# Performance work log

Hardware: AMD Instinct MI355X
Metric: run time of the kernel (lower is better)

Reference implementation:

```python
import jax, jax.numpy as jnp
import numpy as np

N_NODES = 50000
N_EDGES = 800000
IN_C, HID_C, OUT_C = 128, 128, 1


def setup_inputs() -> dict:
    key = jax.random.key(0)
    ks = jax.random.split(key, 10)
    x = jax.random.normal(ks[0], (N_NODES, IN_C), dtype=jnp.float32)
    x2 = jax.random.normal(ks[1], (1,), dtype=jnp.float32)
    edge_index = jax.random.randint(ks[2], (2, N_EDGES), 0, N_NODES, dtype=jnp.int64)
    # GCNConv params (glorot-ish scale) and final linear
    W1 = jax.random.normal(ks[3], (IN_C, HID_C), dtype=jnp.float32) / np.sqrt(IN_C)
    b1 = jnp.zeros((HID_C,), dtype=jnp.float32)
    W2 = jax.random.normal(ks[4], (HID_C, HID_C), dtype=jnp.float32) / np.sqrt(HID_C)
    b2 = jnp.zeros((HID_C,), dtype=jnp.float32)
    Wlin = jax.random.normal(ks[5], (HID_C, OUT_C), dtype=jnp.float32) / np.sqrt(HID_C)
    blin = jnp.zeros((OUT_C,), dtype=jnp.float32)
    return {"x": x, "x2": x2, "edge_index": edge_index, "num_nodes": N_NODES,
            "W1": W1, "b1": b1, "W2": W2, "b2": b2, "Wlin": Wlin, "blin": blin}


def _gcn_conv(h, W, b, src, dst, norm, num_nodes):
    # linear transform then normalized scatter-add aggregation (PyG GCNConv)
    h = h @ W  # [N, C_out]
    msg = h[src] * norm[:, None]  # gather + scale, [E+N, C_out]
    out = jax.ops.segment_sum(msg, dst, num_segments=num_nodes)
    return out + b


def _gcn_norm(edge_index, num_nodes):
    # add self-loops, compute sym-normalization coefficients D^-1/2 A D^-1/2
    loop = jnp.arange(num_nodes, dtype=edge_index.dtype)
    src = jnp.concatenate([edge_index[0], loop])
    dst = jnp.concatenate([edge_index[1], loop])
    ones = jnp.ones(src.shape[0], dtype=jnp.float32)
    deg = jax.ops.segment_sum(ones, dst, num_segments=num_nodes)
    dinv = jnp.where(deg > 0, jax.lax.rsqrt(deg), 0.0)
    norm = dinv[src] * dinv[dst]
    return src, dst, norm


def reference(x, x2, edge_index, num_nodes, W1, b1, W2, b2, Wlin, blin):
    src, dst, norm = _gcn_norm(edge_index, num_nodes)
    h = _gcn_conv(x, W1, b1, src, dst, norm, num_nodes)
    h = jax.nn.relu(h)
    # dropout is identity in eval mode
    h = _gcn_conv(h, W2, b2, src, dst, norm, num_nodes)
    h = jax.nn.relu(h)
    out = h @ Wlin + blin  # [N, 1]
    return out.squeeze(-1)
```

## Files before the change

### kernel.cpp

```cpp
#include <hip/hip_runtime.h>
#include <hip/hip_bf16.h>

#define N_NODES 50000
#define N_EDGES 800000
#define C 128

#define NBB   391
#define CAPB  2600
#define CHUNK 2048

__global__ __launch_bounds__(256) void k_binA(const int* __restrict__ ei,
                                              int* __restrict__ gcur,
                                              int2* __restrict__ tmp) {
    __shared__ int hist[NBB];
    __shared__ int lbase[NBB];
    __shared__ int gbaseL[NBB];
    __shared__ int stmp[256];
    __shared__ int2 buf[CHUNK];
    __shared__ int totalv;

    int tid = threadIdx.x;
    int e0 = blockIdx.x * CHUNK;

    for (int i = tid; i < NBB; i += 256) hist[i] = 0;
    __syncthreads();

    int sarr[8], darr[8], parr[8];
#pragma unroll
    for (int j = 0; j < 8; ++j) {
        int e = e0 + j * 256 + tid;
        darr[j] = -1;
        if (e < N_EDGES) {
            sarr[j] = ei[e];
            int d = ei[N_EDGES + e];
            darr[j] = d;
            parr[j] = atomicAdd(&hist[d >> 7], 1);
        }
    }
    __syncthreads();

    {
        int i0 = 2 * tid, i1 = 2 * tid + 1;
        int c0 = (i0 < NBB) ? hist[i0] : 0;
        int c1 = (i1 < NBB) ? hist[i1] : 0;
        int c = c0 + c1;
        stmp[tid] = c;
        __syncthreads();
        int v = c;
        for (int d = 1; d < 256; d <<= 1) {
            int w = (tid >= d) ? stmp[tid - d] : 0;
            __syncthreads();
            v += w;
            stmp[tid] = v;
            __syncthreads();
        }
        int excl = v - c;
        if (i0 < NBB) lbase[i0] = excl;
        if (i1 < NBB) lbase[i1] = excl + c0;
        if (tid == 255) totalv = v;
    }
    for (int i = tid; i < NBB; i += 256) {
        int cnt = hist[i];
        int run = (cnt > 0) ? atomicAdd(&gcur[i], cnt) : 0;
        gbaseL[i] = i * CAPB + run;
    }
    __syncthreads();

#pragma unroll
    for (int j = 0; j < 8; ++j) {
        if (darr[j] >= 0) {
            int b = darr[j] >> 7;
            buf[lbase[b] + parr[j]] = make_int2(sarr[j], darr[j]);
        }
    }
    __syncthreads();

    int total = totalv;
    for (int i = tid; i < total; i += 256) {
        int2 v = buf[i];
        int b = v.y >> 7;
        int gpos = gbaseL[b] + (i - lbase[b]);
        if (gpos < (b + 1) * CAPB) tmp[gpos] = v;
    }
}

__global__ __launch_bounds__(256) void k_dinv(const int2* __restrict__ tmp,
                                              const int* __restrict__ gcur,
                                              float* __restrict__ dinv) {
    __shared__ int cnt[128];
    int b = blockIdx.x, tid = threadIdx.x;
    if (tid < 128) cnt[tid] = 0;
    __syncthreads();
    int n = gcur[b];
    if (n > CAPB) n = CAPB;
    for (int i = tid; i < n; i += 256)
        atomicAdd(&cnt[tmp[b * CAPB + i].y & 127], 1);
    __syncthreads();
    int node = b * 128 + tid;
    if (tid < 128 && node < N_NODES)
        dinv[node] = rsqrtf((float)cnt[tid] + 1.0f);
}

__device__ __forceinline__ unsigned int bf16rtn(float f) {
    unsigned int u = __float_as_uint(f);
    return (u + 0x7fffu + ((u >> 16) & 1u)) >> 16;
}
__device__ __forceinline__ unsigned int packbf2(float lo, float hi) {
    return bf16rtn(lo) | (bf16rtn(hi) << 16);
}

#define XS_STRIDE 44

template <bool RELU>
__global__ __launch_bounds__(256, 2) void k_gemm(const float* __restrict__ A,
                                                 const float* __restrict__ W,
                                                 const float* __restrict__ dinv,
                                                 unsigned int* __restrict__ Hout) {
    __shared__ float Wp[32 * 128];
    __shared__ float Xs[64 * XS_STRIDE];
    int tid = threadIdx.x;
    int cg = tid & 15;
    int rg = tid >> 4;
    int row0 = blockIdx.x * 64;

    const float4* W4 = (const float4*)W;
    const float4* A4 = (const float4*)A;
    float4* Wp4 = (float4*)Wp;

    float4 acc[4][2];
#pragma unroll
    for (int i = 0; i < 4; ++i) {
        acc[i][0] = make_float4(0.f, 0.f, 0.f, 0.f);
        acc[i][1] = make_float4(0.f, 0.f, 0.f, 0.f);
    }

    for (int p = 0; p < 4; ++p) {
        if (p) __syncthreads();
#pragma unroll
        for (int i = 0; i < 4; ++i)
            Wp4[tid + 256 * i] = W4[p * 1024 + tid + 256 * i];
#pragma unroll
        for (int i = 0; i < 2; ++i) {
            int idx = tid + 256 * i;
            int r = idx >> 3, c4 = idx & 7;
            int gr = row0 + r;
            float4 v = make_float4(0.f, 0.f, 0.f, 0.f);
            if (gr < N_NODES) v = A4[gr * 32 + p * 8 + c4];
            if (RELU) {
                v.x = fmaxf(v.x, 0.f); v.y = fmaxf(v.y, 0.f);
                v.z = fmaxf(v.z, 0.f); v.w = fmaxf(v.w, 0.f);
            }
            *(float4*)(Xs + r * XS_STRIDE + c4 * 4) = v;
        }
        __syncthreads();

#pragma unroll
        for (int k0 = 0; k0 < 32; k0 += 4) {
            float4 wv[4][2];
#pragma unroll
            for (int kk = 0; kk < 4; ++kk) {
                wv[kk][0] = Wp4[(k0 + kk) * 32 + cg];
                wv[kk][1] = Wp4[(k0 + kk) * 32 + 16 + cg];
            }
            float4 xv[4];
#pragma unroll
            for (int i = 0; i < 4; ++i)
                xv[i] = *(const float4*)(Xs + (rg * 4 + i) * XS_STRIDE + k0);
#pragma unroll
            for (int i = 0; i < 4; ++i) {
#pragma unroll
                for (int kk = 0; kk < 4; ++kk) {
                    float xs = (kk == 0) ? xv[i].x : (kk == 1) ? xv[i].y
                             : (kk == 2) ? xv[i].z : xv[i].w;
#pragma unroll
                    for (int h = 0; h < 2; ++h) {
                        acc[i][h].x += xs * wv[kk][h].x;
                        acc[i][h].y += xs * wv[kk][h].y;
                        acc[i][h].z += xs * wv[kk][h].z;
                        acc[i][h].w += xs * wv[kk][h].w;
                    }
                }
            }
        }
    }

#pragma unroll
    for (int i = 0; i < 4; ++i) {
        int gr = row0 + rg * 4 + i;
        if (gr < N_NODES) {
            float dv = dinv[gr];
            uint2 u0, u1;
            u0.x = packbf2(dv * acc[i][0].x, dv * acc[i][0].y);
            u0.y = packbf2(dv * acc[i][0].z, dv * acc[i][0].w);
            u1.x = packbf2(dv * acc[i][1].x, dv * acc[i][1].y);
            u1.y = packbf2(dv * acc[i][1].z, dv * acc[i][1].w);
            *(uint2*)&Hout[gr * 64 + cg * 2]      = u0;
            *(uint2*)&Hout[gr * 64 + 32 + cg * 2] = u1;
        }
    }
}

__device__ __forceinline__ void add8(float* acc, uint4 u) {
    acc[0] += __uint_as_float(u.x << 16);
    acc[1] += __uint_as_float(u.x & 0xffff0000u);
    acc[2] += __uint_as_float(u.y << 16);
    acc[3] += __uint_as_float(u.y & 0xffff0000u);
    acc[4] += __uint_as_float(u.z << 16);
    acc[5] += __uint_as_float(u.z & 0xffff0000u);
    acc[6] += __uint_as_float(u.w << 16);
    acc[7] += __uint_as_float(u.w & 0xffff0000u);
}

template <bool FINAL>
__global__ __launch_bounds__(1024) void k_agg(const uint4* __restrict__ h4,
                                              const int2* __restrict__ tmp,
                                              const int* __restrict__ gcur,
                                              const float* __restrict__ bias,
                                              const float* __restrict__ Wlin,
                                              const float* __restrict__ blin,
                                              float* __restrict__ aggout) {
    __shared__ int   rawsrc[CAPB];
    __shared__ short rawloc[CAPB];
    __shared__ int   lcsr[CAPB];
    __shared__ int   lcnt[128];
    __shared__ int   lbase0[128];
    __shared__ int   lcur[128];
    __shared__ int   stmp[128];

    int b = blockIdx.x, tid = threadIdx.x;
    int cnt = gcur[b];
    if (cnt > CAPB) cnt = CAPB;

    if (tid < 128) { lcnt[tid] = 0; lcur[tid] = 0; }
    __syncthreads();

    for (int i = tid; i < cnt; i += 1024) {
        int2 v = tmp[b * CAPB + i];
        int l = v.y & 127;
        rawsrc[i] = v.x;
        rawloc[i] = (short)l;
        atomicAdd(&lcnt[l], 1);
    }
    __syncthreads();

    {
        int c = (tid < 128) ? lcnt[tid] : 0;
        if (tid < 128) stmp[tid] = c;
        __syncthreads();
        int v = c;
        for (int d = 1; d < 128; d <<= 1) {
            int w = (tid >= d && tid < 128) ? stmp[tid - d] : 0;
            __syncthreads();
            if (tid < 128) { v += w; stmp[tid] = v; }
            __syncthreads();
        }
        if (tid < 128) lbase0[tid] = v - c;
    }
    __syncthreads();

    for (int i = tid; i < cnt; i += 1024) {
        int l = rawloc[i];
        int p = atomicAdd(&lcur[l], 1);
        lcsr[lbase0[l] + p] = rawsrc[i];
    }
    __syncthreads();

    int wv = tid >> 6, lane = tid & 63, eg = lane >> 4, cq = lane & 15;

    float4 bv0 = ((const float4*)bias)[cq * 2];
    float4 bv1 = ((const float4*)bias)[cq * 2 + 1];
    float4 wl0 = make_float4(0.f, 0.f, 0.f, 0.f), wl1 = wl0;
    float bl = 0.f;
    if (FINAL) {
        wl0 = ((const float4*)Wlin)[cq * 2];
        wl1 = ((const float4*)Wlin)[cq * 2 + 1];
        bl = blin[0];
    }

#pragma unroll 1
    for (int t = 0; t < 8; ++t) {
        int ln = wv * 8 + t;
        int node = b * 128 + ln;
        if (node >= N_NODES) break;
        int deg = lcnt[ln];
        int o0 = lbase0[ln], o1 = o0 + deg;

        float acc[8];
#pragma unroll
        for (int j = 0; j < 8; ++j) acc[j] = 0.f;

        int e = o0;
        for (; e + 8 <= o1; e += 8) {
            int s0 = lcsr[e + 2 * eg];
            int s1 = lcsr[e + 2 * eg + 1];
            uint4 u0 = h4[s0 * 16 + cq];
            uint4 u1 = h4[s1 * 16 + cq];
            add8(acc, u0);
            add8(acc, u1);
        }
        {
            int r = o1 - e;
            int b0 = e + 2 * eg;
            if (2 * eg < r)     { int s = lcsr[b0];     add8(acc, h4[s * 16 + cq]); }
            if (2 * eg + 1 < r) { int s = lcsr[b0 + 1]; add8(acc, h4[s * 16 + cq]); }
        }
#pragma unroll
        for (int j = 0; j < 8; ++j) {
            acc[j] += __shfl_xor(acc[j], 16, 64);
            acc[j] += __shfl_xor(acc[j], 32, 64);
        }

        float dv = rsqrtf((float)deg + 1.0f);
        uint4 us = h4[node * 16 + cq];
        float hv[8];
        hv[0] = __uint_as_float(us.x << 16); hv[1] = __uint_as_float(us.x & 0xffff0000u);
        hv[2] = __uint_as_float(us.y << 16); hv[3] = __uint_as_float(us.y & 0xffff0000u);
        hv[4] = __uint_as_float(us.z << 16); hv[5] = __uint_as_float(us.z & 0xffff0000u);
        hv[6] = __uint_as_float(us.w << 16); hv[7] = __uint_as_float(us.w & 0xffff0000u);
        float o[8];
        o[0] = dv * (acc[0] + hv[0]) + bv0.x;
        o[1] = dv * (acc[1] + hv[1]) + bv0.y;
        o[2] = dv * (acc[2] + hv[2]) + bv0.z;
        o[3] = dv * (acc[3] + hv[3]) + bv0.w;
        o[4] = dv * (acc[4] + hv[4]) + bv1.x;
        o[5] = dv * (acc[5] + hv[5]) + bv1.y;
        o[6] = dv * (acc[6] + hv[6]) + bv1.z;
        o[7] = dv * (acc[7] + hv[7]) + bv1.w;

        if (!FINAL) {
            if (eg == 0) {
                float4* out4 = (float4*)aggout;
                out4[node * 32 + cq * 2]     = make_float4(o[0], o[1], o[2], o[3]);
                out4[node * 32 + cq * 2 + 1] = make_float4(o[4], o[5], o[6], o[7]);
            }
        } else {
            float v = fmaxf(o[0], 0.f) * wl0.x + fmaxf(o[1], 0.f) * wl0.y
                    + fmaxf(o[2], 0.f) * wl0.z + fmaxf(o[3], 0.f) * wl0.w
                    + fmaxf(o[4], 0.f) * wl1.x + fmaxf(o[5], 0.f) * wl1.y
                    + fmaxf(o[6], 0.f) * wl1.z + fmaxf(o[7], 0.f) * wl1.w;
            v += __shfl_xor(v, 1, 64);
            v += __shfl_xor(v, 2, 64);
            v += __shfl_xor(v, 4, 64);
            v += __shfl_xor(v, 8, 64);
            if (lane == 0) aggout[node] = v + bl;
        }
    }
}

extern "C" void kernel_launch(void* const* d_in, const int* in_sizes, int n_in,
                              void* d_out, int out_size, void* d_ws, size_t ws_size,
                              hipStream_t stream) {
    const float* x    = (const float*)d_in[0];
    const int*   ei   = (const int*)d_in[2];
    const float* W1   = (const float*)d_in[4];
    const float* b1   = (const float*)d_in[5];
    const float* W2   = (const float*)d_in[6];
    const float* b2   = (const float*)d_in[7];
    const float* Wlin = (const float*)d_in[8];
    const float* blin = (const float*)d_in[9];
    float* out = (float*)d_out;

    char* ws = (char*)d_ws;
    size_t off = 0;
    auto carve = [&](size_t bytes) -> void* {
        void* p = ws + off;
        off = (off + bytes + 255) & ~(size_t)255;
        return p;
    };
    int*   gcur = (int*)  carve(NBB * sizeof(int));
    float* dinv = (float*)carve(N_NODES * sizeof(float));
    int2*  tmp  = (int2*) carve((size_t)NBB * CAPB * sizeof(int2));
    unsigned int* hbf = (unsigned int*)carve((size_t)N_NODES * 64 * sizeof(unsigned int));
    float* agg  = (float*)carve((size_t)N_NODES * C * sizeof(float));

    const int NB_A = (N_EDGES + CHUNK - 1) / CHUNK;
    const int NB_G = (N_NODES + 63) / 64;

    hipMemsetAsync(gcur, 0, NBB * sizeof(int), stream);

    k_binA<<<NB_A, 256, 0, stream>>>(ei, gcur, tmp);
    k_dinv<<<NBB, 256, 0, stream>>>(tmp, gcur, dinv);

    k_gemm<false><<<NB_G, 256, 0, stream>>>(x, W1, dinv, hbf);
    k_agg<false><<<NBB, 1024, 0, stream>>>((const uint4*)hbf, tmp, gcur,
                                           b1, Wlin, blin, agg);
    k_gemm<true><<<NB_G, 256, 0, stream>>>(agg, W2, dinv, hbf);
    k_agg<true><<<NBB, 1024, 0, stream>>>((const uint4*)hbf, tmp, gcur,
                                          b2, Wlin, blin, out);
}
```

Measured before the change: 239.4 us.

## Halve GEMM row tile and register-prefetch next W/A slice

The dense transform kernel now processes 32 rows per block instead of 64, doubling the grid and raising the occupancy hint from 2 to 5 blocks per CU. It also prefetches the next K-slice of W and A into registers while the current slice is computed from shared memory, overlapping global loads with FMA work. In exchange, each block's W-slice load is amortised over half as many rows, so global W traffic per row doubles.

```diff
diff --git a/kernel.cpp b/kernel.cpp
--- a/kernel.cpp
+++ b/kernel.cpp
@@ -109,50 +109,64 @@
     return bf16rtn(lo) | (bf16rtn(hi) << 16);
 }
 
-#define XS_STRIDE 44
+#define XT_STRIDE 36
 
 template <bool RELU>
-__global__ __launch_bounds__(256, 2) void k_gemm(const float* __restrict__ A,
+__global__ __launch_bounds__(256, 5) void k_gemm(const float* __restrict__ A,
                                                  const float* __restrict__ W,
                                                  const float* __restrict__ dinv,
                                                  unsigned int* __restrict__ Hout) {
     __shared__ float Wp[32 * 128];
-    __shared__ float Xs[64 * XS_STRIDE];
+    __shared__ float Xs[32 * XT_STRIDE];
     int tid = threadIdx.x;
     int cg = tid & 15;
     int rg = tid >> 4;
-    int row0 = blockIdx.x * 64;
+    int row0 = blockIdx.x * 32;
 
     const float4* W4 = (const float4*)W;
     const float4* A4 = (const float4*)A;
     float4* Wp4 = (float4*)Wp;
 
-    float4 acc[4][2];
-#pragma unroll
-    for (int i = 0; i < 4; ++i) {
+    int ar = tid >> 3;
+    int ac = tid & 7;
+    int gr_a = row0 + ar;
+
+    float4 acc[2][2];
+#pragma unroll
+    for (int i = 0; i < 2; ++i) {
         acc[i][0] = make_float4(0.f, 0.f, 0.f, 0.f);
         acc[i][1] = make_float4(0.f, 0.f, 0.f, 0.f);
     }
 
+    float4 wst[4];
+    float4 ast;
+#pragma unroll
+    for (int i = 0; i < 4; ++i) wst[i] = W4[tid + 256 * i];
+    {
+        float4 v = make_float4(0.f, 0.f, 0.f, 0.f);
+        if (gr_a < N_NODES) v = A4[gr_a * 32 + ac];
+        ast = v;
+    }
+
+#pragma unroll 1
     for (int p = 0; p < 4; ++p) {
         if (p) __syncthreads();
-#pragma unroll
-        for (int i = 0; i < 4; ++i)
-            Wp4[tid + 256 * i] = W4[p * 1024 + tid + 256 * i];
-#pragma unroll
-        for (int i = 0; i < 2; ++i) {
-            int idx = tid + 256 * i;
-            int r = idx >> 3, c4 = idx & 7;
-            int gr = row0 + r;
+        if (RELU) {
+            ast.x = fmaxf(ast.x, 0.f); ast.y = fmaxf(ast.y, 0.f);
+            ast.z = fmaxf(ast.z, 0.f); ast.w = fmaxf(ast.w, 0.f);
+        }
+#pragma unroll
+        for (int i = 0; i < 4; ++i) Wp4[tid + 256 * i] = wst[i];
+        *(float4*)(Xs + ar * XT_STRIDE + ac * 4) = ast;
+        __syncthreads();
+
+        if (p < 3) {
+#pragma unroll
+            for (int i = 0; i < 4; ++i) wst[i] = W4[(p + 1) * 1024 + tid + 256 * i];
             float4 v = make_float4(0.f, 0.f, 0.f, 0.f);
-            if (gr < N_NODES) v = A4[gr * 32 + p * 8 + c4];
-            if (RELU) {
-                v.x = fmaxf(v.x, 0.f); v.y = fmaxf(v.y, 0.f);
-                v.z = fmaxf(v.z, 0.f); v.w = fmaxf(v.w, 0.f);
-            }
-            *(float4*)(Xs + r * XS_STRIDE + c4 * 4) = v;
-        }
-        __syncthreads();
+            if (gr_a < N_NODES) v = A4[gr_a * 32 + (p + 1) * 8 + ac];
+            ast = v;
+        }
 
 #pragma unroll
         for (int k0 = 0; k0 < 32; k0 += 4) {
@@ -162,12 +176,12 @@
                 wv[kk][0] = Wp4[(k0 + kk) * 32 + cg];
                 wv[kk][1] = Wp4[(k0 + kk) * 32 + 16 + cg];
             }
-            float4 xv[4];
-#pragma unroll
-            for (int i = 0; i < 4; ++i)
-                xv[i] = *(const float4*)(Xs + (rg * 4 + i) * XS_STRIDE + k0);
-#pragma unroll
-            for (int i = 0; i < 4; ++i) {
+            float4 xv[2];
+#pragma unroll
+            for (int i = 0; i < 2; ++i)
+                xv[i] = *(const float4*)(Xs + (rg * 2 + i) * XT_STRIDE + k0);
+#pragma unroll
+            for (int i = 0; i < 2; ++i) {
 #pragma unroll
                 for (int kk = 0; kk < 4; ++kk) {
                     float xs = (kk == 0) ? xv[i].x : (kk == 1) ? xv[i].y
@@ -185,8 +199,8 @@
     }
 
 #pragma unroll
-    for (int i = 0; i < 4; ++i) {
-        int gr = row0 + rg * 4 + i;
+    for (int i = 0; i < 2; ++i) {
+        int gr = row0 + rg * 2 + i;
         if (gr < N_NODES) {
             float dv = dinv[gr];
             uint2 u0, u1;
@@ -374,7 +388,7 @@
     float* agg  = (float*)carve((size_t)N_NODES * C * sizeof(float));
 
     const int NB_A = (N_EDGES + CHUNK - 1) / CHUNK;
-    const int NB_G = (N_NODES + 63) / 64;
+    const int NB_G = (N_NODES + 31) / 32;
 
     hipMemsetAsync(gcur, 0, NBB * sizeof(int), stream);
 
```

Result: slower. 289.1 us (+20.8%).

## Use bf16 MFMA with split-precision weights for node feature GEMMs

Applied to the files above, without the earlier changes.

Replaces the scalar FP32 register-tiled GEMM with a matrix-core kernel using mfma_f32_16x16x32_bf16. Activations are rounded to bf16 in swizzled LDS, and weights are split into high and low bf16 parts by a new prep kernel, so two MFMAs per step keep weight precision. This removes the FP32 FMA cost of the dense transforms but lowers activation precision to bf16 and adds a small extra kernel launch.

```diff
diff --git a/kernel.cpp b/kernel.cpp
--- a/kernel.cpp
+++ b/kernel.cpp
@@ -8,6 +8,9 @@
 #define NBB   391
 #define CAPB  2600
 #define CHUNK 2048
+
+typedef __attribute__((ext_vector_type(8))) short short8v;
+typedef __attribute__((ext_vector_type(4))) float f32x4;
 
 __global__ __launch_bounds__(256) void k_binA(const int* __restrict__ ei,
                                               int* __restrict__ gcur,
@@ -109,93 +112,108 @@
     return bf16rtn(lo) | (bf16rtn(hi) << 16);
 }
 
-#define XS_STRIDE 44
+__global__ void k_prepW(const float* __restrict__ W1, const float* __restrict__ W2,
+                        unsigned short* __restrict__ Wsplit) {
+    int t = blockIdx.x * 256 + threadIdx.x;
+    if (t >= 32768) return;
+    int layer = t >> 14, idx = t & 16383;
+    int i = idx >> 7, j = idx & 127;
+    const float* Wsrc = layer ? W2 : W1;
+    float w = Wsrc[i * 128 + j];
+    unsigned int h = bf16rtn(w);
+    float hf = __uint_as_float(h << 16);
+    unsigned int l = bf16rtn(w - hf);
+    unsigned short* base = Wsplit + layer * 32768;
+    base[j * 128 + i] = (unsigned short)h;
+    base[16384 + j * 128 + i] = (unsigned short)l;
+}
 
 template <bool RELU>
-__global__ __launch_bounds__(256, 2) void k_gemm(const float* __restrict__ A,
-                                                 const float* __restrict__ W,
+__global__ __launch_bounds__(512, 4) void k_gemm(const float* __restrict__ A,
+                                                 const unsigned short* __restrict__ Whg,
+                                                 const unsigned short* __restrict__ Wlg,
                                                  const float* __restrict__ dinv,
-                                                 unsigned int* __restrict__ Hout) {
-    __shared__ float Wp[32 * 128];
-    __shared__ float Xs[64 * XS_STRIDE];
+                                                 unsigned short* __restrict__ Hout) {
+    __shared__ uint4 Al[64 * 16];
+    __shared__ float ddv[64];
+
     int tid = threadIdx.x;
-    int cg = tid & 15;
-    int rg = tid >> 4;
     int row0 = blockIdx.x * 64;
-
-    const float4* W4 = (const float4*)W;
-    const float4* A4 = (const float4*)A;
-    float4* Wp4 = (float4*)Wp;
-
-    float4 acc[4][2];
-#pragma unroll
-    for (int i = 0; i < 4; ++i) {
-        acc[i][0] = make_float4(0.f, 0.f, 0.f, 0.f);
-        acc[i][1] = make_float4(0.f, 0.f, 0.f, 0.f);
-    }
-
-    for (int p = 0; p < 4; ++p) {
-        if (p) __syncthreads();
-#pragma unroll
-        for (int i = 0; i < 4; ++i)
-            Wp4[tid + 256 * i] = W4[p * 1024 + tid + 256 * i];
-#pragma unroll
-        for (int i = 0; i < 2; ++i) {
-            int idx = tid + 256 * i;
-            int r = idx >> 3, c4 = idx & 7;
-            int gr = row0 + r;
-            float4 v = make_float4(0.f, 0.f, 0.f, 0.f);
-            if (gr < N_NODES) v = A4[gr * 32 + p * 8 + c4];
-            if (RELU) {
-                v.x = fmaxf(v.x, 0.f); v.y = fmaxf(v.y, 0.f);
-                v.z = fmaxf(v.z, 0.f); v.w = fmaxf(v.w, 0.f);
+    int wv = tid >> 6, lane = tid & 63;
+    int col = wv * 16 + (lane & 15);
+    int kq = lane >> 4;
+
+    const uint4* Bh4 = (const uint4*)Whg;
+    const uint4* Bl4 = (const uint4*)Wlg;
+    short8v bh[4], bl[4];
+#pragma unroll
+    for (int ks = 0; ks < 4; ++ks) {
+        uint4 uh = Bh4[col * 16 + ks * 4 + kq];
+        uint4 ul = Bl4[col * 16 + ks * 4 + kq];
+        bh[ks] = *reinterpret_cast<short8v*>(&uh);
+        bl[ks] = *reinterpret_cast<short8v*>(&ul);
+    }
+
+#pragma unroll
+    for (int pass = 0; pass < 2; ++pass) {
+        int row = (tid >> 4) + pass * 32;
+        int o = tid & 15;
+        int gr = row0 + row;
+        float4 v0 = make_float4(0.f, 0.f, 0.f, 0.f), v1 = v0;
+        if (gr < N_NODES) {
+            const float4* A4 = (const float4*)A;
+            v0 = A4[gr * 32 + o * 2];
+            v1 = A4[gr * 32 + o * 2 + 1];
+        }
+        if (RELU) {
+            v0.x = fmaxf(v0.x, 0.f); v0.y = fmaxf(v0.y, 0.f);
+            v0.z = fmaxf(v0.z, 0.f); v0.w = fmaxf(v0.w, 0.f);
+            v1.x = fmaxf(v1.x, 0.f); v1.y = fmaxf(v1.y, 0.f);
+            v1.z = fmaxf(v1.z, 0.f); v1.w = fmaxf(v1.w, 0.f);
+        }
+        uint4 u;
+        u.x = packbf2(v0.x, v0.y);
+        u.y = packbf2(v0.z, v0.w);
+        u.z = packbf2(v1.x, v1.y);
+        u.w = packbf2(v1.z, v1.w);
+        int byte = (row * 256 + o * 16) ^ ((row & 7) << 4);
+        Al[byte >> 4] = u;
+    }
+    if (tid < 64) {
+        int gr = row0 + tid;
+        ddv[tid] = (gr < N_NODES) ? dinv[gr] : 0.f;
+    }
+    __syncthreads();
+
+    f32x4 acc[4];
+#pragma unroll
+    for (int st = 0; st < 4; ++st) acc[st] = (f32x4){0.f, 0.f, 0.f, 0.f};
+
+#pragma unroll
+    for (int st = 0; st < 4; ++st) {
+        int rowl = st * 16 + (lane & 15);
+        int rbase = rowl * 256;
+        int swz = (rowl & 7) << 4;
+#pragma unroll
+        for (int ks = 0; ks < 4; ++ks) {
+            int byte = (rbase + ks * 64 + kq * 16) ^ swz;
+            uint4 ua = Al[byte >> 4];
+            short8v a = *reinterpret_cast<short8v*>(&ua);
+            acc[st] = __builtin_amdgcn_mfma_f32_16x16x32_bf16(a, bh[ks], acc[st], 0, 0, 0);
+            acc[st] = __builtin_amdgcn_mfma_f32_16x16x32_bf16(a, bl[ks], acc[st], 0, 0, 0);
+        }
+    }
+
+#pragma unroll
+    for (int st = 0; st < 4; ++st) {
+#pragma unroll
+        for (int r = 0; r < 4; ++r) {
+            int rowl = st * 16 + kq * 4 + r;
+            int gr = row0 + rowl;
+            if (gr < N_NODES) {
+                float dv = ddv[rowl];
+                Hout[gr * 128 + col] = (unsigned short)bf16rtn(dv * acc[st][r]);
             }
-            *(float4*)(Xs + r * XS_STRIDE + c4 * 4) = v;
-        }
-        __syncthreads();
-
-#pragma unroll
-        for (int k0 = 0; k0 < 32; k0 += 4) {
-            float4 wv[4][2];
-#pragma unroll
-            for (int kk = 0; kk < 4; ++kk) {
-                wv[kk][0] = Wp4[(k0 + kk) * 32 + cg];
-                wv[kk][1] = Wp4[(k0 + kk) * 32 + 16 + cg];
-            }
-            float4 xv[4];
-#pragma unroll
-            for (int i = 0; i < 4; ++i)
-                xv[i] = *(const float4*)(Xs + (rg * 4 + i) * XS_STRIDE + k0);
-#pragma unroll
-            for (int i = 0; i < 4; ++i) {
-#pragma unroll
-                for (int kk = 0; kk < 4; ++kk) {
-                    float xs = (kk == 0) ? xv[i].x : (kk == 1) ? xv[i].y
-                             : (kk == 2) ? xv[i].z : xv[i].w;
-#pragma unroll
-                    for (int h = 0; h < 2; ++h) {
-                        acc[i][h].x += xs * wv[kk][h].x;
-                        acc[i][h].y += xs * wv[kk][h].y;
-                        acc[i][h].z += xs * wv[kk][h].z;
-                        acc[i][h].w += xs * wv[kk][h].w;
-                    }
-                }
-            }
-        }
-    }
-
-#pragma unroll
-    for (int i = 0; i < 4; ++i) {
-        int gr = row0 + rg * 4 + i;
-        if (gr < N_NODES) {
-            float dv = dinv[gr];
-            uint2 u0, u1;
-            u0.x = packbf2(dv * acc[i][0].x, dv * acc[i][0].y);
-            u0.y = packbf2(dv * acc[i][0].z, dv * acc[i][0].w);
-            u1.x = packbf2(dv * acc[i][1].x, dv * acc[i][1].y);
-            u1.y = packbf2(dv * acc[i][1].z, dv * acc[i][1].w);
-            *(uint2*)&Hout[gr * 64 + cg * 2]      = u0;
-            *(uint2*)&Hout[gr * 64 + 32 + cg * 2] = u1;
         }
     }
 }
@@ -370,21 +388,28 @@
     int*   gcur = (int*)  carve(NBB * sizeof(int));
     float* dinv = (float*)carve(N_NODES * sizeof(float));
     int2*  tmp  = (int2*) carve((size_t)NBB * CAPB * sizeof(int2));
-    unsigned int* hbf = (unsigned int*)carve((size_t)N_NODES * 64 * sizeof(unsigned int));
+    unsigned short* hbf = (unsigned short*)carve((size_t)N_NODES * C * sizeof(unsigned short));
     float* agg  = (float*)carve((size_t)N_NODES * C * sizeof(float));
+    unsigned short* wsplit = (unsigned short*)carve(4 * 16384 * sizeof(unsigned short));
 
     const int NB_A = (N_EDGES + CHUNK - 1) / CHUNK;
     const int NB_G = (N_NODES + 63) / 64;
 
     hipMemsetAsync(gcur, 0, NBB * sizeof(int), stream);
 
+    k_prepW<<<128, 256, 0, stream>>>(W1, W2, wsplit);
     k_binA<<<NB_A, 256, 0, stream>>>(ei, gcur, tmp);
     k_dinv<<<NBB, 256, 0, stream>>>(tmp, gcur, dinv);
 
-    k_gemm<false><<<NB_G, 256, 0, stream>>>(x, W1, dinv, hbf);
+    const unsigned short* W1h = wsplit;
+    const unsigned short* W1l = wsplit + 16384;
+    const unsigned short* W2h = wsplit + 32768;
+    const unsigned short* W2l = wsplit + 49152;
+
+    k_gemm<false><<<NB_G, 512, 0, stream>>>(x, W1h, W1l, dinv, hbf);
     k_agg<false><<<NBB, 1024, 0, stream>>>((const uint4*)hbf, tmp, gcur,
                                            b1, Wlin, blin, agg);
-    k_gemm<true><<<NB_G, 256, 0, stream>>>(agg, W2, dinv, hbf);
+    k_gemm<true><<<NB_G, 512, 0, stream>>>(agg, W2h, W2l, dinv, hbf);
     k_agg<true><<<NBB, 1024, 0, stream>>>((const uint4*)hbf, tmp, gcur,
                                           b2, Wlin, blin, out);
 }
```

New measurement: 202.0 us. 1.19x faster.
